# Kernel tuning notes

Measured on AMD Instinct MI355X. Metric: run time of the kernel, lower is better.

Reference implementation:

```python
import jax, jax.numpy as jnp
import numpy as np

B, T, U, V, H, KA, KO = 64, 600, 64, 80, 512, 10, 20


def setup_inputs() -> dict:
    key = jax.random.key(0)
    ks = jax.random.split(key, 12)
    std = 0.075
    p = lambda k, shape: jax.random.normal(k, shape, jnp.float32) * std
    return dict(
        char_seq=jax.random.randint(ks[0], (B, U), 0, V),
        char_mask=jnp.ones((B, U), jnp.float32),
        strokes=jax.random.normal(ks[1], (B, T, 3), jnp.float32),
        strokes_mask=jnp.ones((B, T), jnp.float32),
        lstm0_Wih=p(ks[2], (4 * H, 3 + V)), lstm0_Whh=p(ks[3], (4 * H, H)), lstm0_b=jnp.zeros((4 * H,), jnp.float32),
        win_W=p(ks[4], (3 * KA, H)), win_b=jnp.zeros((3 * KA,), jnp.float32),
        lstm1_Wih=p(ks[5], (4 * H, 3 + V + H)), lstm1_Whh=p(ks[6], (4 * H, H)), lstm1_b=jnp.zeros((4 * H,), jnp.float32),
        lstm2_Wih=p(ks[7], (4 * H, 3 + V + H)), lstm2_Whh=p(ks[8], (4 * H, H)), lstm2_b=jnp.zeros((4 * H,), jnp.float32),
        fc_W=p(ks[9], (6 * KO + 1, 3 * H)), fc_b=jnp.zeros((6 * KO + 1,), jnp.float32),
    )


def _lstm_cell(gates_x, h, c, Whh):
    # gates_x already contains x@Wih.T + b; PyTorch gate order: i, f, g, o
    gates = gates_x + h @ Whh.T
    i, f, g, o = jnp.split(gates, 4, axis=-1)
    c = jax.nn.sigmoid(f) * c + jax.nn.sigmoid(i) * jnp.tanh(g)
    h = jax.nn.sigmoid(o) * jnp.tanh(c)
    return h, c


def _run_lstm(x, Wih, Whh, b):
    # x: [B, T, F]; precompute input projection once (big GEMM), scan only on h.
    gx = jnp.einsum('btf,gf->btg', x, Wih) + b  # [B,T,4H]
    h0 = jnp.zeros((x.shape[0], H), x.dtype)
    c0 = jnp.zeros((x.shape[0], H), x.dtype)

    def step(carry, g_t):
        h, c = carry
        h, c = _lstm_cell(g_t, h, c, Whh)
        return (h, c), h

    _, hs = jax.lax.scan(step, (h0, c0), gx.transpose(1, 0, 2))
    return hs.transpose(1, 0, 2)  # [B,T,H]


def _forward(char_seq, char_mask, strokes,
             lstm0_Wih, lstm0_Whh, lstm0_b, win_W, win_b,
             lstm1_Wih, lstm1_Whh, lstm1_b, lstm2_Wih, lstm2_Whh, lstm2_b,
             fc_W, fc_b):
    char_oh = jax.nn.one_hot(char_seq, V, dtype=jnp.float32) * char_mask[..., None]  # [B,U,V]
    u_grid = jnp.arange(U, dtype=jnp.float32)  # char positions

    h0 = jnp.zeros((B, H), jnp.float32)
    c0 = jnp.zeros((B, H), jnp.float32)
    w0 = jnp.zeros((B, V), jnp.float32)
    k0 = jnp.zeros((B, KA), jnp.float32)

    def step(carry, x_t):
        h, c, w, k = carry
        inp = jnp.concatenate([x_t, w], axis=-1)  # [B, 3+V]
        gates = inp @ lstm0_Wih.T + lstm0_b
        h, c = _lstm_cell(gates, h, c, lstm0_Whh)
        # Gaussian attention window (Graves 2013)
        p = h @ win_W.T + win_b  # [B, 3K]
        alpha, beta, kap_hat = jnp.split(jnp.exp(p), 3, axis=-1)
        k = k + kap_hat  # [B,K]
        phi = jnp.sum(alpha[:, :, None] * jnp.exp(-beta[:, :, None] * (k[:, :, None] - u_grid) ** 2), axis=1)
        phi = phi * char_mask  # [B,U]
        w = jnp.einsum('bu,buv->bv', phi, char_oh)
        return (h, c, w, k), (h, w)

    _, (h_seq, w_seq) = jax.lax.scan(step, (h0, c0, w0, k0), strokes.transpose(1, 0, 2))
    lstm0_out = h_seq.transpose(1, 0, 2)   # [B,T,H]
    attn_out = w_seq.transpose(1, 0, 2)    # [B,T,V]

    lstm1_out = _run_lstm(jnp.concatenate([strokes, attn_out, lstm0_out], -1), lstm1_Wih, lstm1_Whh, lstm1_b)
    lstm2_out = _run_lstm(jnp.concatenate([strokes, attn_out, lstm1_out], -1), lstm2_Wih, lstm2_Whh, lstm2_b)

    final = jnp.einsum('bth,gh->btg', jnp.concatenate([lstm0_out, lstm1_out, lstm2_out], -1), fc_W) + fc_b
    # parse_outputs: split [2K, 2K, K, K, 1]
    myu = final[..., : 2 * KO]
    log_sigma = final[..., 2 * KO: 4 * KO]
    pi = final[..., 4 * KO: 5 * KO]
    rho = final[..., 5 * KO: 6 * KO]
    eos = final[..., 6 * KO:]
    log_pi = jax.nn.log_softmax(pi, axis=-1)
    rho = jnp.tanh(rho)
    eos = jax.nn.sigmoid(-eos)
    myu = myu.reshape(myu.shape[:-1] + (KO, 2))
    log_sigma = log_sigma.reshape(log_sigma.shape[:-1] + (KO, 2))
    return (log_pi, myu, log_sigma, rho, eos)


def reference(char_seq, char_mask, strokes, strokes_mask,
              lstm0_Wih, lstm0_Whh, lstm0_b, win_W, win_b,
              lstm1_Wih, lstm1_Whh, lstm1_b, lstm2_Wih, lstm2_Whh, lstm2_b,
              fc_W, fc_b):
    # strokes_mask is unused by forward() in the original module (only in losses)
    return _forward(char_seq, char_mask, strokes,
                    lstm0_Wih, lstm0_Whh, lstm0_b, win_W, win_b,
                    lstm1_Wih, lstm1_Whh, lstm1_b, lstm2_Wih, lstm2_Whh, lstm2_b,
                    fc_W, fc_b)
```

## Files before the change

### kernel.cpp

```cpp
#include <hip/hip_runtime.h>
#include <hip/hip_bf16.h>
#include <math.h>

#define B_ 64
#define T_ 600
#define U_ 64
#define V_ 80
#define H_ 512
#define KA_ 10
#define KO_ 20

__device__ __forceinline__ float sigmf(float x){ return 1.0f/(1.0f+expf(-x)); }

__global__ __launch_bounds__(256) void k_lstm3(
    int tau,
    const float* __restrict__ strokes,
    const float* attn_t,
    const float* __restrict__ W0ih, const float* __restrict__ W0hh, const float* __restrict__ b0,
    const float* __restrict__ W1ih, const float* __restrict__ W1hh, const float* __restrict__ b1,
    const float* __restrict__ W2ih, const float* __restrict__ W2hh, const float* __restrict__ b2,
    float* out0, float* out1, float* out2,
    float* c0, float* c1, float* c2)
{
    int layer = blockIdx.x >> 8;
    int wg    = blockIdx.x & 255;
    int t     = tau - layer;
    if (t < 0 || t >= T_) return;

    const float* Wih; const float* Whh; const float* bias;
    const float* xprev; float* outp; float* cst; int Lx; int astep;
    if (layer == 0){ Wih=W0ih; Whh=W0hh; bias=b0; xprev=nullptr; outp=out0; cst=c0; Lx=3+V_;     astep=t-1; }
    else if (layer == 1){ Wih=W1ih; Whh=W1hh; bias=b1; xprev=out0; outp=out1; cst=c1; Lx=3+V_+H_; astep=t; }
    else { Wih=W2ih; Whh=W2hh; bias=b2; xprev=out1; outp=out2; cst=c2; Lx=3+V_+H_; astep=t; }

    int tid = threadIdx.x;
    int b   = tid & 63;
    int sl  = tid >> 6;
    int jl  = sl & 1;
    int ks  = sl >> 1;
    int j   = wg*2 + jl;

    float acc0=0.f, acc1=0.f, acc2=0.f, acc3=0.f;

    if (ks == 0){
        const float* w0 = Wih + (size_t)(0*H_+j)*Lx;
        const float* w1 = Wih + (size_t)(1*H_+j)*Lx;
        const float* w2 = Wih + (size_t)(2*H_+j)*Lx;
        const float* w3 = Wih + (size_t)(3*H_+j)*Lx;
        const float* sr = strokes + ((size_t)b*T_ + t)*3;
        float x0=sr[0], x1=sr[1], x2=sr[2];
        acc0 = x0*w0[0] + x1*w0[1] + x2*w0[2];
        acc1 = x0*w1[0] + x1*w1[1] + x2*w1[2];
        acc2 = x0*w2[0] + x1*w2[1] + x2*w2[2];
        acc3 = x0*w3[0] + x1*w3[1] + x2*w3[2];
        if (astep >= 0){
            const float* ap = attn_t + (size_t)astep*V_*B_ + b;
            #pragma unroll 8
            for (int v=0; v<V_; ++v){
                float av = ap[(size_t)v*B_];
                acc0 += av*w0[3+v]; acc1 += av*w1[3+v]; acc2 += av*w2[3+v]; acc3 += av*w3[3+v];
            }
        }
        if (xprev){
            const float* xp = xprev + (size_t)t*H_*B_ + b;
            #pragma unroll 8
            for (int k=0; k<H_; ++k){
                float xv = xp[(size_t)k*B_];
                acc0 += xv*w0[83+k]; acc1 += xv*w1[83+k]; acc2 += xv*w2[83+k]; acc3 += xv*w3[83+k];
            }
        }
    } else {
        if (t > 0){
            const float* hp = outp + (size_t)(t-1)*H_*B_ + b;
            const float4* r0 = (const float4*)(Whh + (size_t)(0*H_+j)*H_);
            const float4* r1 = (const float4*)(Whh + (size_t)(1*H_+j)*H_);
            const float4* r2 = (const float4*)(Whh + (size_t)(2*H_+j)*H_);
            const float4* r3 = (const float4*)(Whh + (size_t)(3*H_+j)*H_);
            #pragma unroll 4
            for (int k=0; k<H_; k+=4){
                float h0 = hp[(size_t)(k+0)*B_];
                float h1 = hp[(size_t)(k+1)*B_];
                float h2 = hp[(size_t)(k+2)*B_];
                float h3 = hp[(size_t)(k+3)*B_];
                float4 q0 = r0[k>>2], q1 = r1[k>>2], q2 = r2[k>>2], q3 = r3[k>>2];
                acc0 += h0*q0.x + h1*q0.y + h2*q0.z + h3*q0.w;
                acc1 += h0*q1.x + h1*q1.y + h2*q1.z + h3*q1.w;
                acc2 += h0*q2.x + h1*q2.y + h2*q2.z + h3*q2.w;
                acc3 += h0*q3.x + h1*q3.y + h2*q3.z + h3*q3.w;
            }
        }
    }

    __shared__ float part[4][4][64];
    part[sl][0][b]=acc0; part[sl][1][b]=acc1; part[sl][2][b]=acc2; part[sl][3][b]=acc3;
    __syncthreads();

    if (sl < 2){
        int jj = wg*2 + sl;
        float gi = part[sl][0][b] + part[sl+2][0][b] + bias[0*H_+jj];
        float gf = part[sl][1][b] + part[sl+2][1][b] + bias[1*H_+jj];
        float gg = part[sl][2][b] + part[sl+2][2][b] + bias[2*H_+jj];
        float go = part[sl][3][b] + part[sl+2][3][b] + bias[3*H_+jj];
        float cold = (t==0) ? 0.f : cst[(size_t)jj*B_+b];
        float cnew = sigmf(gf)*cold + sigmf(gi)*tanhf(gg);
        cst[(size_t)jj*B_+b] = cnew;
        outp[((size_t)t*H_+jj)*B_+b] = sigmf(go)*tanhf(cnew);
    }
}

__global__ __launch_bounds__(64) void k_window(
    int t,
    const float* out0, const float* __restrict__ winW, const float* __restrict__ winb,
    const int* __restrict__ char_seq, const float* __restrict__ char_mask,
    float* attn_t, float* kst)
{
    int b = blockIdx.x; int tid = threadIdx.x;
    __shared__ float sa[KA_], sb_[KA_], sk[KA_], sphi[U_];
    __shared__ int   sseq[U_];
    __shared__ float smask[U_];

    sseq[tid]  = char_seq[b*U_+tid];
    smask[tid] = char_mask[b*U_+tid];

    if (tid < 3*KA_){
        const float* hrow = out0 + (size_t)t*H_*B_ + b;
        const float* wr   = winW + (size_t)tid*H_;
        float p = winb[tid];
        #pragma unroll 8
        for (int k=0; k<H_; ++k) p += hrow[(size_t)k*B_]*wr[k];
        float e = expf(p);
        if (tid < KA_) sa[tid] = e;
        else if (tid < 2*KA_) sb_[tid-KA_] = e;
        else {
            int a = tid - 2*KA_;
            float kn = ((t==0) ? 0.f : kst[a*B_+b]) + e;
            kst[a*B_+b] = kn;
            sk[a] = kn;
        }
    }
    __syncthreads();

    {
        int u = tid;
        float acc = 0.f;
        #pragma unroll
        for (int a=0; a<KA_; ++a){
            float d = sk[a] - (float)u;
            acc += sa[a]*expf(-sb_[a]*d*d);
        }
        sphi[u] = acc * smask[u] * smask[u];
    }
    __syncthreads();

    for (int v=tid; v<V_; v+=64){
        float wv = 0.f;
        for (int u=0; u<U_; ++u) wv += (sseq[u]==v) ? sphi[u] : 0.f;
        attn_t[((size_t)t*V_+v)*B_+b] = wv;
    }
}

__global__ __launch_bounds__(256) void k_fc(
    const float* out0, const float* out1, const float* out2,
    const float* __restrict__ fcW, const float* __restrict__ fcb, float* finalb)
{
    int t = blockIdx.x; int tid = threadIdx.x;
    int b = tid & 63; int gq = tid >> 6;
    __shared__ float acts[128][B_];
    float acc[31];
    #pragma unroll
    for (int i=0; i<31; ++i) acc[i] = 0.f;

    const float* outs[3] = {out0, out1, out2};
    for (int seg=0; seg<3; ++seg){
        const float* o = outs[seg] + (size_t)t*H_*B_;
        for (int kc=0; kc<H_; kc+=128){
            __syncthreads();
            for (int i=tid; i<128*B_; i+=256){
                int k = i>>6, bb = i&63;
                acts[k][bb] = o[(size_t)(kc+k)*B_ + bb];
            }
            __syncthreads();
            for (int kk=0; kk<128; ++kk){
                float a = acts[kk][b];
                int K = seg*H_ + kc + kk;
                #pragma unroll
                for (int i=0; i<30; ++i)
                    acc[i] += a * fcW[(size_t)(gq+4*i)*1536 + K];
                if (gq == 0)
                    acc[30] += a * fcW[(size_t)120*1536 + K];
            }
        }
    }
    for (int i=0; i<30; ++i){
        int g = gq + 4*i;
        finalb[((size_t)t*121+g)*B_+b] = acc[i] + fcb[g];
    }
    if (gq == 0)
        finalb[((size_t)t*121+120)*B_+b] = acc[30] + fcb[120];
}

__global__ __launch_bounds__(256) void k_transform(const float* __restrict__ finalb, float* __restrict__ out)
{
    int idx = blockIdx.x*256 + threadIdx.x;
    int t = idx >> 6; int b = idx & 63;
    const float* f = finalb + (size_t)t*121*B_ + b;
    size_t bt = (size_t)b*T_ + t;

    float* myu = out + 768000;
    #pragma unroll
    for (int i=0; i<40; ++i) myu[bt*40 + i] = f[(size_t)i*B_];

    float* lsg = out + 2304000;
    #pragma unroll
    for (int i=0; i<40; ++i) lsg[bt*40 + i] = f[(size_t)(40+i)*B_];

    float pi[KO_];
    float m = -1e30f;
    #pragma unroll
    for (int ko=0; ko<KO_; ++ko){ pi[ko] = f[(size_t)(80+ko)*B_]; m = fmaxf(m, pi[ko]); }
    float s = 0.f;
    #pragma unroll
    for (int ko=0; ko<KO_; ++ko) s += expf(pi[ko]-m);
    float lse = m + logf(s);
    #pragma unroll
    for (int ko=0; ko<KO_; ++ko) out[bt*20 + ko] = pi[ko] - lse;

    float* rho = out + 3840000;
    #pragma unroll
    for (int ko=0; ko<KO_; ++ko) rho[bt*20 + ko] = tanhf(f[(size_t)(100+ko)*B_]);

    out[4608000 + bt] = 1.f/(1.f + expf(f[(size_t)120*B_]));
}

extern "C" void kernel_launch(void* const* d_in, const int* in_sizes, int n_in,
                              void* d_out, int out_size, void* d_ws, size_t ws_size,
                              hipStream_t stream)
{
    const int*   char_seq  = (const int*)  d_in[0];
    const float* char_mask = (const float*)d_in[1];
    const float* strokes   = (const float*)d_in[2];
    const float* W0ih = (const float*)d_in[4];
    const float* W0hh = (const float*)d_in[5];
    const float* b0   = (const float*)d_in[6];
    const float* winW = (const float*)d_in[7];
    const float* winb = (const float*)d_in[8];
    const float* W1ih = (const float*)d_in[9];
    const float* W1hh = (const float*)d_in[10];
    const float* b1   = (const float*)d_in[11];
    const float* W2ih = (const float*)d_in[12];
    const float* W2hh = (const float*)d_in[13];
    const float* b2   = (const float*)d_in[14];
    const float* fcW  = (const float*)d_in[15];
    const float* fcb  = (const float*)d_in[16];

    float* ws    = (float*)d_ws;
    float* out0  = ws;
    float* out1  = out0 + 19660800;
    float* out2  = out1 + 19660800;
    float* attn  = out2 + 19660800;
    float* c0    = attn + 3072000;
    float* c1    = c0 + 32768;
    float* c2    = c1 + 32768;
    float* kst   = c2 + 32768;
    float* finalb= kst + 640;

    for (int tau=0; tau<T_+2; ++tau){
        hipLaunchKernelGGL(k_lstm3, dim3(768), dim3(256), 0, stream, tau,
            strokes, attn, W0ih, W0hh, b0, W1ih, W1hh, b1, W2ih, W2hh, b2,
            out0, out1, out2, c0, c1, c2);
        if (tau < T_)
            hipLaunchKernelGGL(k_window, dim3(64), dim3(64), 0, stream, tau,
                out0, winW, winb, char_seq, char_mask, attn, kst);
    }
    hipLaunchKernelGGL(k_fc, dim3(600), dim3(256), 0, stream, out0, out1, out2, fcW, fcb, finalb);
    hipLaunchKernelGGL(k_transform, dim3(150), dim3(256), 0, stream, finalb, (float*)d_out);
}
```

Measured before the change: 52.37 ms.

## Replace per-step kernel launches with persistent pipelined kernel using atomic flags

Replaces the 1200+ per-timestep launches with one persistent kernel of 448 blocks: 384 LSTM blocks (three layers) and 64 attention-window blocks. They coordinate through acquire/release counters in global memory, so layers and the window pipeline across timesteps without returning to the host. Weights are repacked once into padded, concatenated rows so every input uses float4 loads, and activations are stored in a float4-interleaved layout. The FC kernel is fused with the output transform. The cost is that correctness and progress rely on all 448 blocks being resident at once, and blocks spend time spin-waiting.

```diff
diff --git a/kernel.cpp b/kernel.cpp
--- a/kernel.cpp
+++ b/kernel.cpp
@@ -1,5 +1,4 @@
 #include <hip/hip_runtime.h>
-#include <hip/hip_bf16.h>
 #include <math.h>
 
 #define B_ 64
@@ -10,226 +9,339 @@
 #define KA_ 10
 #define KO_ 20
 
+#define S0_ 600
+#define S12_ 1108
+
 __device__ __forceinline__ float sigmf(float x){ return 1.0f/(1.0f+expf(-x)); }
 
-__global__ __launch_bounds__(256) void k_lstm3(
-    int tau,
+__device__ __forceinline__ void spin_ge(int* p, int target){
+    while (__hip_atomic_load(p, __ATOMIC_ACQUIRE, __HIP_MEMORY_SCOPE_AGENT) < target){
+        __builtin_amdgcn_s_sleep(2);
+    }
+}
+
+__device__ __forceinline__ void flag_add(int* p){
+    __hip_atomic_fetch_add(p, 1, __ATOMIC_RELEASE, __HIP_MEMORY_SCOPE_AGENT);
+}
+
+#define BLOCK_WAIT(p, tgt) do { if (threadIdx.x == 0) spin_ge((p), (tgt)); __syncthreads(); } while (0)
+
+__global__ __launch_bounds__(64) void k_prep(
+    const float* __restrict__ W0ih, const float* __restrict__ W0hh,
+    const float* __restrict__ W1ih, const float* __restrict__ W1hh,
+    const float* __restrict__ W2ih, const float* __restrict__ W2hh,
+    float* __restrict__ wpad)
+{
+    int r = blockIdx.x;
+    int tid = threadIdx.x;
+    if (r < 2048){
+        float* dst = wpad + (size_t)r*S0_;
+        const float* sih = W0ih + (size_t)r*83;
+        const float* shh = W0hh + (size_t)r*512;
+        if (tid < 3) dst[tid] = sih[tid];
+        if (tid == 3) dst[3] = 0.f;
+        for (int v=tid; v<V_; v+=64) dst[4+v] = sih[3+v];
+        for (int k=tid; k<H_; k+=64) dst[84+k] = shh[k];
+    } else {
+        int rr = r - 2048;
+        int layer = rr >> 11;
+        int row = rr & 2047;
+        const float* sih = (layer==0 ? W1ih : W2ih) + (size_t)row*595;
+        const float* shh = (layer==0 ? W1hh : W2hh) + (size_t)row*512;
+        float* dst = wpad + (size_t)2048*S0_ + ((size_t)layer*2048 + row)*S12_;
+        if (tid < 3) dst[tid] = sih[tid];
+        if (tid == 3) dst[3] = 0.f;
+        for (int v=tid; v<V_; v+=64) dst[4+v] = sih[3+v];
+        for (int k=tid; k<H_; k+=64) dst[84+k] = sih[83+k];
+        for (int k=tid; k<H_; k+=64) dst[596+k] = shh[k];
+    }
+}
+
+__global__ __launch_bounds__(256, 2) void k_pipe(
     const float* __restrict__ strokes,
-    const float* attn_t,
-    const float* __restrict__ W0ih, const float* __restrict__ W0hh, const float* __restrict__ b0,
-    const float* __restrict__ W1ih, const float* __restrict__ W1hh, const float* __restrict__ b1,
-    const float* __restrict__ W2ih, const float* __restrict__ W2hh, const float* __restrict__ b2,
-    float* out0, float* out1, float* out2,
-    float* c0, float* c1, float* c2)
+    const int*   __restrict__ char_seq,
+    const float* __restrict__ char_mask,
+    const float* __restrict__ wpad,
+    const float* __restrict__ winW, const float* __restrict__ winb,
+    const float* __restrict__ b0, const float* __restrict__ b1, const float* __restrict__ b2,
+    float* __restrict__ out0, float* __restrict__ out1, float* __restrict__ out2,
+    float* __restrict__ attn, int* __restrict__ sync)
 {
-    int layer = blockIdx.x >> 8;
-    int wg    = blockIdx.x & 255;
-    int t     = tau - layer;
-    if (t < 0 || t >= T_) return;
-
-    const float* Wih; const float* Whh; const float* bias;
-    const float* xprev; float* outp; float* cst; int Lx; int astep;
-    if (layer == 0){ Wih=W0ih; Whh=W0hh; bias=b0; xprev=nullptr; outp=out0; cst=c0; Lx=3+V_;     astep=t-1; }
-    else if (layer == 1){ Wih=W1ih; Whh=W1hh; bias=b1; xprev=out0; outp=out1; cst=c1; Lx=3+V_+H_; astep=t; }
-    else { Wih=W2ih; Whh=W2hh; bias=b2; xprev=out1; outp=out2; cst=c2; Lx=3+V_+H_; astep=t; }
-
-    int tid = threadIdx.x;
-    int b   = tid & 63;
-    int sl  = tid >> 6;
-    int jl  = sl & 1;
-    int ks  = sl >> 1;
-    int j   = wg*2 + jl;
-
-    float acc0=0.f, acc1=0.f, acc2=0.f, acc3=0.f;
-
-    if (ks == 0){
-        const float* w0 = Wih + (size_t)(0*H_+j)*Lx;
-        const float* w1 = Wih + (size_t)(1*H_+j)*Lx;
-        const float* w2 = Wih + (size_t)(2*H_+j)*Lx;
-        const float* w3 = Wih + (size_t)(3*H_+j)*Lx;
-        const float* sr = strokes + ((size_t)b*T_ + t)*3;
-        float x0=sr[0], x1=sr[1], x2=sr[2];
-        acc0 = x0*w0[0] + x1*w0[1] + x2*w0[2];
-        acc1 = x0*w1[0] + x1*w1[1] + x2*w1[2];
-        acc2 = x0*w2[0] + x1*w2[1] + x2*w2[2];
-        acc3 = x0*w3[0] + x1*w3[1] + x2*w3[2];
-        if (astep >= 0){
-            const float* ap = attn_t + (size_t)astep*V_*B_ + b;
-            #pragma unroll 8
-            for (int v=0; v<V_; ++v){
-                float av = ap[(size_t)v*B_];
-                acc0 += av*w0[3+v]; acc1 += av*w1[3+v]; acc2 += av*w2[3+v]; acc3 += av*w3[3+v];
-            }
-        }
-        if (xprev){
-            const float* xp = xprev + (size_t)t*H_*B_ + b;
-            #pragma unroll 8
-            for (int k=0; k<H_; ++k){
-                float xv = xp[(size_t)k*B_];
-                acc0 += xv*w0[83+k]; acc1 += xv*w1[83+k]; acc2 += xv*w2[83+k]; acc3 += xv*w3[83+k];
-            }
-        }
-    } else {
-        if (t > 0){
-            const float* hp = outp + (size_t)(t-1)*H_*B_ + b;
-            const float4* r0 = (const float4*)(Whh + (size_t)(0*H_+j)*H_);
-            const float4* r1 = (const float4*)(Whh + (size_t)(1*H_+j)*H_);
-            const float4* r2 = (const float4*)(Whh + (size_t)(2*H_+j)*H_);
-            const float4* r3 = (const float4*)(Whh + (size_t)(3*H_+j)*H_);
-            #pragma unroll 4
-            for (int k=0; k<H_; k+=4){
-                float h0 = hp[(size_t)(k+0)*B_];
-                float h1 = hp[(size_t)(k+1)*B_];
-                float h2 = hp[(size_t)(k+2)*B_];
-                float h3 = hp[(size_t)(k+3)*B_];
-                float4 q0 = r0[k>>2], q1 = r1[k>>2], q2 = r2[k>>2], q3 = r3[k>>2];
-                acc0 += h0*q0.x + h1*q0.y + h2*q0.z + h3*q0.w;
-                acc1 += h0*q1.x + h1*q1.y + h2*q1.z + h3*q1.w;
-                acc2 += h0*q2.x + h1*q2.y + h2*q2.z + h3*q2.w;
-                acc3 += h0*q3.x + h1*q3.y + h2*q3.z + h3*q3.w;
-            }
-        }
-    }
+    int* c0 = sync;
+    int* c1 = sync + 640;
+    int* c2 = sync + 1280;
+    int* cw = sync + 1920;
+
+    const int bid = blockIdx.x;
+    const int tid = threadIdx.x;
+    const int b   = tid & 63;
+    const int g   = tid >> 6;
 
     __shared__ float part[4][4][64];
-    part[sl][0][b]=acc0; part[sl][1][b]=acc1; part[sl][2][b]=acc2; part[sl][3][b]=acc3;
-    __syncthreads();
-
-    if (sl < 2){
-        int jj = wg*2 + sl;
-        float gi = part[sl][0][b] + part[sl+2][0][b] + bias[0*H_+jj];
-        float gf = part[sl][1][b] + part[sl+2][1][b] + bias[1*H_+jj];
-        float gg = part[sl][2][b] + part[sl+2][2][b] + bias[2*H_+jj];
-        float go = part[sl][3][b] + part[sl+2][3][b] + bias[3*H_+jj];
-        float cold = (t==0) ? 0.f : cst[(size_t)jj*B_+b];
-        float cnew = sigmf(gf)*cold + sigmf(gi)*tanhf(gg);
-        cst[(size_t)jj*B_+b] = cnew;
-        outp[((size_t)t*H_+jj)*B_+b] = sigmf(go)*tanhf(cnew);
-    }
-}
-
-__global__ __launch_bounds__(64) void k_window(
-    int t,
-    const float* out0, const float* __restrict__ winW, const float* __restrict__ winb,
-    const int* __restrict__ char_seq, const float* __restrict__ char_mask,
-    float* attn_t, float* kst)
-{
-    int b = blockIdx.x; int tid = threadIdx.x;
-    __shared__ float sa[KA_], sb_[KA_], sk[KA_], sphi[U_];
+    __shared__ float pp[30][8];
+    __shared__ float sa[KA_], sbv[KA_], sk[KA_], skst[KA_];
+    __shared__ float sphi[U_];
     __shared__ int   sseq[U_];
     __shared__ float smask[U_];
 
-    sseq[tid]  = char_seq[b*U_+tid];
-    smask[tid] = char_mask[b*U_+tid];
-
-    if (tid < 3*KA_){
-        const float* hrow = out0 + (size_t)t*H_*B_ + b;
-        const float* wr   = winW + (size_t)tid*H_;
-        float p = winb[tid];
-        #pragma unroll 8
-        for (int k=0; k<H_; ++k) p += hrow[(size_t)k*B_]*wr[k];
-        float e = expf(p);
-        if (tid < KA_) sa[tid] = e;
-        else if (tid < 2*KA_) sb_[tid-KA_] = e;
-        else {
-            int a = tid - 2*KA_;
-            float kn = ((t==0) ? 0.f : kst[a*B_+b]) + e;
-            kst[a*B_+b] = kn;
-            sk[a] = kn;
-        }
-    }
-    __syncthreads();
-
-    {
-        int u = tid;
-        float acc = 0.f;
-        #pragma unroll
-        for (int a=0; a<KA_; ++a){
-            float d = sk[a] - (float)u;
-            acc += sa[a]*expf(-sb_[a]*d*d);
-        }
-        sphi[u] = acc * smask[u] * smask[u];
-    }
-    __syncthreads();
-
-    for (int v=tid; v<V_; v+=64){
-        float wv = 0.f;
-        for (int u=0; u<U_; ++u) wv += (sseq[u]==v) ? sphi[u] : 0.f;
-        attn_t[((size_t)t*V_+v)*B_+b] = wv;
+    if (bid >= 384){
+        const int wb = bid - 384;
+        if (tid < U_){ sseq[tid] = char_seq[wb*U_+tid]; smask[tid] = char_mask[wb*U_+tid]; }
+        __syncthreads();
+        for (int t=0; t<T_; ++t){
+            BLOCK_WAIT(&c0[t], 128);
+            if (t >= 8){
+                BLOCK_WAIT(&c1[t-8], 128);
+                BLOCK_WAIT(&c2[t-8], 128);
+            }
+            if (tid < 240){
+                int r = tid >> 3, p8 = tid & 7;
+                const float4* hp = (const float4*)(out0 + (size_t)t*32768);
+                const float4* wr = (const float4*)(winW + (size_t)r*H_);
+                float acc = 0.f;
+                int kq0 = p8*16;
+                #pragma unroll 4
+                for (int i=0; i<16; ++i){
+                    float4 xv = hp[(size_t)(kq0+i)*64 + wb];
+                    float4 wv = wr[kq0+i];
+                    acc += xv.x*wv.x + xv.y*wv.y + xv.z*wv.z + xv.w*wv.w;
+                }
+                pp[r][p8] = acc;
+            }
+            __syncthreads();
+            if (tid < 30){
+                float p = winb[tid];
+                #pragma unroll
+                for (int i=0; i<8; ++i) p += pp[tid][i];
+                float e = expf(p);
+                if (tid < KA_) sa[tid] = e;
+                else if (tid < 2*KA_) sbv[tid-KA_] = e;
+                else {
+                    int a2 = tid - 2*KA_;
+                    float kn = ((t == 0) ? 0.f : skst[a2]) + e;
+                    skst[a2] = kn; sk[a2] = kn;
+                }
+            }
+            __syncthreads();
+            if (tid < U_){
+                float acc = 0.f;
+                #pragma unroll
+                for (int a=0; a<KA_; ++a){
+                    float d = sk[a] - (float)tid;
+                    acc += sa[a]*expf(-sbv[a]*d*d);
+                }
+                sphi[tid] = acc * smask[tid]*smask[tid];
+            }
+            __syncthreads();
+            if (tid < V_){
+                float wv = 0.f;
+                for (int u=0; u<U_; ++u) wv += (sseq[u] == tid) ? sphi[u] : 0.f;
+                attn[(size_t)(t&7)*5120 + (size_t)(tid>>2)*256 + wb*4 + (tid&3)] = wv;
+            }
+            __syncthreads();
+            if (tid == 0) flag_add(&cw[t]);
+        }
+        return;
+    }
+
+    const int l  = bid >> 7;
+    const int ub = (bid & 127) * 4;
+
+    const float* wbase; const float* bias_p; const float* xprev; float* outp;
+    int* cself; int* cprev; size_t wstride; int roff;
+    if (l == 0){ wbase = wpad;                                          wstride = S0_;  bias_p = b0; outp = out0; xprev = nullptr; cself = c0; cprev = nullptr; roff = 84; }
+    else if (l == 1){ wbase = wpad + (size_t)2048*S0_;                  wstride = S12_; bias_p = b1; outp = out1; xprev = out0;   cself = c1; cprev = c0;     roff = 596; }
+    else { wbase = wpad + (size_t)2048*S0_ + (size_t)2048*S12_;         wstride = S12_; bias_p = b2; outp = out2; xprev = out1;   cself = c2; cprev = c1;     roff = 596; }
+
+    const float* wr = wbase + ((size_t)g*H_ + ub)*wstride;
+    const float* wr1 = wr + wstride;
+    const float* wr2 = wr + 2*wstride;
+    const float* wr3 = wr + 3*wstride;
+
+    const int cu = ub + g;
+    const float bgi = bias_p[0*H_+cu];
+    const float bgf = bias_p[1*H_+cu];
+    const float bgg = bias_p[2*H_+cu];
+    const float bgo = bias_p[3*H_+cu];
+    float creg = 0.f;
+
+    for (int t=0; t<T_; ++t){
+        float a0, a1, a2, a3;
+        {
+            const float* sr = strokes + ((size_t)b*T_ + t)*3;
+            float sx=sr[0], sy=sr[1], sz=sr[2];
+            a0 = sx*wr[0]  + sy*wr[1]  + sz*wr[2];
+            a1 = sx*wr1[0] + sy*wr1[1] + sz*wr1[2];
+            a2 = sx*wr2[0] + sy*wr2[1] + sz*wr2[2];
+            a3 = sx*wr3[0] + sy*wr3[1] + sz*wr3[2];
+        }
+        if (t > 0){
+            BLOCK_WAIT(&cself[t-1], 128);
+            const float4* hp = (const float4*)(outp + (size_t)(t-1)*32768) + b;
+            #pragma unroll 4
+            for (int kq=0; kq<128; ++kq){
+                float4 xv = hp[kq*64];
+                float4 q0 = *(const float4*)(wr  + roff + kq*4);
+                float4 q1 = *(const float4*)(wr1 + roff + kq*4);
+                float4 q2 = *(const float4*)(wr2 + roff + kq*4);
+                float4 q3 = *(const float4*)(wr3 + roff + kq*4);
+                a0 += xv.x*q0.x + xv.y*q0.y + xv.z*q0.z + xv.w*q0.w;
+                a1 += xv.x*q1.x + xv.y*q1.y + xv.z*q1.z + xv.w*q1.w;
+                a2 += xv.x*q2.x + xv.y*q2.y + xv.z*q2.z + xv.w*q2.w;
+                a3 += xv.x*q3.x + xv.y*q3.y + xv.z*q3.z + xv.w*q3.w;
+            }
+        }
+        if (l > 0){
+            BLOCK_WAIT(&cprev[t], 128);
+            const float4* hp = (const float4*)(xprev + (size_t)t*32768) + b;
+            #pragma unroll 4
+            for (int kq=0; kq<128; ++kq){
+                float4 xv = hp[kq*64];
+                float4 q0 = *(const float4*)(wr  + 84 + kq*4);
+                float4 q1 = *(const float4*)(wr1 + 84 + kq*4);
+                float4 q2 = *(const float4*)(wr2 + 84 + kq*4);
+                float4 q3 = *(const float4*)(wr3 + 84 + kq*4);
+                a0 += xv.x*q0.x + xv.y*q0.y + xv.z*q0.z + xv.w*q0.w;
+                a1 += xv.x*q1.x + xv.y*q1.y + xv.z*q1.z + xv.w*q1.w;
+                a2 += xv.x*q2.x + xv.y*q2.y + xv.z*q2.z + xv.w*q2.w;
+                a3 += xv.x*q3.x + xv.y*q3.y + xv.z*q3.z + xv.w*q3.w;
+            }
+        }
+        {
+            int ta = (l == 0) ? (t-1) : t;
+            if (ta >= 0){
+                BLOCK_WAIT(&cw[ta], 64);
+                const float4* ap = (const float4*)(attn + (size_t)(ta&7)*5120) + b;
+                #pragma unroll 4
+                for (int vq=0; vq<20; ++vq){
+                    float4 xv = ap[vq*64];
+                    float4 q0 = *(const float4*)(wr  + 4 + vq*4);
+                    float4 q1 = *(const float4*)(wr1 + 4 + vq*4);
+                    float4 q2 = *(const float4*)(wr2 + 4 + vq*4);
+                    float4 q3 = *(const float4*)(wr3 + 4 + vq*4);
+                    a0 += xv.x*q0.x + xv.y*q0.y + xv.z*q0.z + xv.w*q0.w;
+                    a1 += xv.x*q1.x + xv.y*q1.y + xv.z*q1.z + xv.w*q1.w;
+                    a2 += xv.x*q2.x + xv.y*q2.y + xv.z*q2.z + xv.w*q2.w;
+                    a3 += xv.x*q3.x + xv.y*q3.y + xv.z*q3.z + xv.w*q3.w;
+                }
+            }
+        }
+        part[g][0][b] = a0;
+        part[g][1][b] = a1;
+        part[g][2][b] = a2;
+        part[g][3][b] = a3;
+        __syncthreads();
+        {
+            float gi  = part[0][g][b] + bgi;
+            float gf  = part[1][g][b] + bgf;
+            float gg_ = part[2][g][b] + bgg;
+            float go  = part[3][g][b] + bgo;
+            float cold = (t == 0) ? 0.f : creg;
+            float cnew = sigmf(gf)*cold + sigmf(gi)*tanhf(gg_);
+            creg = cnew;
+            float h = sigmf(go)*tanhf(cnew);
+            outp[(size_t)t*32768 + (size_t)(cu>>2)*256 + b*4 + (cu&3)] = h;
+        }
+        __syncthreads();
+        if (tid == 0) flag_add(&cself[t]);
     }
 }
 
 __global__ __launch_bounds__(256) void k_fc(
-    const float* out0, const float* out1, const float* out2,
-    const float* __restrict__ fcW, const float* __restrict__ fcb, float* finalb)
+    const float* __restrict__ out0, const float* __restrict__ out1, const float* __restrict__ out2,
+    const float* __restrict__ fcW, const float* __restrict__ fcb, float* __restrict__ out)
 {
     int t = blockIdx.x; int tid = threadIdx.x;
     int b = tid & 63; int gq = tid >> 6;
-    __shared__ float acts[128][B_];
+    __shared__ float smraw[128*65];
+
     float acc[31];
     #pragma unroll
     for (int i=0; i<31; ++i) acc[i] = 0.f;
 
     const float* outs[3] = {out0, out1, out2};
     for (int seg=0; seg<3; ++seg){
-        const float* o = outs[seg] + (size_t)t*H_*B_;
+        const float* o = outs[seg] + (size_t)t*32768;
         for (int kc=0; kc<H_; kc+=128){
             __syncthreads();
-            for (int i=tid; i<128*B_; i+=256){
-                int k = i>>6, bb = i&63;
-                acts[k][bb] = o[(size_t)(kc+k)*B_ + bb];
-            }
-            __syncthreads();
-            for (int kk=0; kk<128; ++kk){
-                float a = acts[kk][b];
+            #pragma unroll
+            for (int r=0; r<8; ++r){
+                int idx = tid + 256*r;
+                int kql = idx >> 6;
+                int bb  = idx & 63;
+                float4 v = *(const float4*)(o + (size_t)((kc>>2) + kql)*256 + bb*4);
+                smraw[(4*kql+0)*65+bb] = v.x;
+                smraw[(4*kql+1)*65+bb] = v.y;
+                smraw[(4*kql+2)*65+bb] = v.z;
+                smraw[(4*kql+3)*65+bb] = v.w;
+            }
+            __syncthreads();
+            for (int kk=0; kk<128; kk+=4){
+                float a0 = smraw[(kk+0)*65+b];
+                float a1 = smraw[(kk+1)*65+b];
+                float a2 = smraw[(kk+2)*65+b];
+                float a3 = smraw[(kk+3)*65+b];
                 int K = seg*H_ + kc + kk;
                 #pragma unroll
-                for (int i=0; i<30; ++i)
-                    acc[i] += a * fcW[(size_t)(gq+4*i)*1536 + K];
-                if (gq == 0)
-                    acc[30] += a * fcW[(size_t)120*1536 + K];
-            }
-        }
-    }
-    for (int i=0; i<30; ++i){
-        int g = gq + 4*i;
-        finalb[((size_t)t*121+g)*B_+b] = acc[i] + fcb[g];
-    }
-    if (gq == 0)
-        finalb[((size_t)t*121+120)*B_+b] = acc[30] + fcb[120];
-}
-
-__global__ __launch_bounds__(256) void k_transform(const float* __restrict__ finalb, float* __restrict__ out)
-{
-    int idx = blockIdx.x*256 + threadIdx.x;
-    int t = idx >> 6; int b = idx & 63;
-    const float* f = finalb + (size_t)t*121*B_ + b;
-    size_t bt = (size_t)b*T_ + t;
-
-    float* myu = out + 768000;
+                for (int i=0; i<30; ++i){
+                    float4 w = *(const float4*)(fcW + (size_t)(gq+4*i)*1536 + K);
+                    acc[i] += a0*w.x + a1*w.y + a2*w.z + a3*w.w;
+                }
+                if (gq == 0){
+                    float4 w = *(const float4*)(fcW + (size_t)120*1536 + K);
+                    acc[30] += a0*w.x + a1*w.y + a2*w.z + a3*w.w;
+                }
+            }
+        }
+    }
+    __syncthreads();
     #pragma unroll
-    for (int i=0; i<40; ++i) myu[bt*40 + i] = f[(size_t)i*B_];
-
-    float* lsg = out + 2304000;
-    #pragma unroll
-    for (int i=0; i<40; ++i) lsg[bt*40 + i] = f[(size_t)(40+i)*B_];
-
-    float pi[KO_];
-    float m = -1e30f;
-    #pragma unroll
-    for (int ko=0; ko<KO_; ++ko){ pi[ko] = f[(size_t)(80+ko)*B_]; m = fmaxf(m, pi[ko]); }
-    float s = 0.f;
-    #pragma unroll
-    for (int ko=0; ko<KO_; ++ko) s += expf(pi[ko]-m);
-    float lse = m + logf(s);
-    #pragma unroll
-    for (int ko=0; ko<KO_; ++ko) out[bt*20 + ko] = pi[ko] - lse;
-
-    float* rho = out + 3840000;
-    #pragma unroll
-    for (int ko=0; ko<KO_; ++ko) rho[bt*20 + ko] = tanhf(f[(size_t)(100+ko)*B_]);
-
-    out[4608000 + bt] = 1.f/(1.f + expf(f[(size_t)120*B_]));
+    for (int i=0; i<30; ++i) smraw[(gq+4*i)*64 + b] = acc[i] + fcb[gq+4*i];
+    if (gq == 0) smraw[120*64 + b] = acc[30] + fcb[120];
+    __syncthreads();
+
+    if (tid < 64){
+        size_t bt = (size_t)b*T_ + t;
+        float* myu = out + 768000;
+        #pragma unroll
+        for (int q=0; q<10; ++q){
+            float4 v;
+            v.x = smraw[(4*q+0)*64+b]; v.y = smraw[(4*q+1)*64+b];
+            v.z = smraw[(4*q+2)*64+b]; v.w = smraw[(4*q+3)*64+b];
+            *(float4*)(myu + bt*40 + 4*q) = v;
+        }
+        float* lsg = out + 2304000;
+        #pragma unroll
+        for (int q=0; q<10; ++q){
+            float4 v;
+            v.x = smraw[(40+4*q+0)*64+b]; v.y = smraw[(40+4*q+1)*64+b];
+            v.z = smraw[(40+4*q+2)*64+b]; v.w = smraw[(40+4*q+3)*64+b];
+            *(float4*)(lsg + bt*40 + 4*q) = v;
+        }
+        float pi[KO_];
+        float m = -1e30f;
+        #pragma unroll
+        for (int ko=0; ko<KO_; ++ko){ pi[ko] = smraw[(80+ko)*64+b]; m = fmaxf(m, pi[ko]); }
+        float s = 0.f;
+        #pragma unroll
+        for (int ko=0; ko<KO_; ++ko) s += expf(pi[ko]-m);
+        float lse = m + logf(s);
+        #pragma unroll
+        for (int q=0; q<5; ++q){
+            float4 v;
+            v.x = pi[4*q+0]-lse; v.y = pi[4*q+1]-lse; v.z = pi[4*q+2]-lse; v.w = pi[4*q+3]-lse;
+            *(float4*)(out + bt*20 + 4*q) = v;
+        }
+        float* rho = out + 3840000;
+        #pragma unroll
+        for (int q=0; q<5; ++q){
+            float4 v;
+            v.x = tanhf(smraw[(100+4*q+0)*64+b]); v.y = tanhf(smraw[(100+4*q+1)*64+b]);
+            v.z = tanhf(smraw[(100+4*q+2)*64+b]); v.w = tanhf(smraw[(100+4*q+3)*64+b]);
+            *(float4*)(rho + bt*20 + 4*q) = v;
+        }
+        out[4608000 + bt] = 1.f/(1.f + expf(smraw[120*64+b]));
+    }
 }
 
 extern "C" void kernel_launch(void* const* d_in, const int* in_sizes, int n_in,
@@ -253,25 +365,23 @@
     const float* fcW  = (const float*)d_in[15];
     const float* fcb  = (const float*)d_in[16];
 
-    float* ws    = (float*)d_ws;
-    float* out0  = ws;
-    float* out1  = out0 + 19660800;
-    float* out2  = out1 + 19660800;
-    float* attn  = out2 + 19660800;
-    float* c0    = attn + 3072000;
-    float* c1    = c0 + 32768;
-    float* c2    = c1 + 32768;
-    float* kst   = c2 + 32768;
-    float* finalb= kst + 640;
-
-    for (int tau=0; tau<T_+2; ++tau){
-        hipLaunchKernelGGL(k_lstm3, dim3(768), dim3(256), 0, stream, tau,
-            strokes, attn, W0ih, W0hh, b0, W1ih, W1hh, b1, W2ih, W2hh, b2,
-            out0, out1, out2, c0, c1, c2);
-        if (tau < T_)
-            hipLaunchKernelGGL(k_window, dim3(64), dim3(64), 0, stream, tau,
-                out0, winW, winb, char_seq, char_mask, attn, kst);
-    }
-    hipLaunchKernelGGL(k_fc, dim3(600), dim3(256), 0, stream, out0, out1, out2, fcW, fcb, finalb);
-    hipLaunchKernelGGL(k_transform, dim3(150), dim3(256), 0, stream, finalb, (float*)d_out);
-}
+    float* ws   = (float*)d_ws;
+    float* out0 = ws;
+    float* out1 = out0 + 19660800;
+    float* out2 = out1 + 19660800;
+    float* attn = out2 + 19660800;
+    float* wpad = attn + 40960;
+    int*   sync = (int*)(wpad + 5767168);
+
+    hipMemsetAsync(sync, 0, 2560*sizeof(int), stream);
+
+    hipLaunchKernelGGL(k_prep, dim3(6144), dim3(64), 0, stream,
+        W0ih, W0hh, W1ih, W1hh, W2ih, W2hh, wpad);
+
+    hipLaunchKernelGGL(k_pipe, dim3(448), dim3(256), 0, stream,
+        strokes, char_seq, char_mask, wpad, winW, winb, b0, b1, b2,
+        out0, out1, out2, attn, sync);
+
+    hipLaunchKernelGGL(k_fc, dim3(600), dim3(256), 0, stream,
+        out0, out1, out2, fcW, fcb, (float*)d_out);
+}
```

After: 187.8 ms. 3.58x slower.
